# Kernel tuning notes

Hardware: AMD Instinct MI355X
Metric: run time of the kernel (lower is better)

Reference implementation:

```python
import jax, jax.numpy as jnp
import numpy as np

N_EMBD = 768
N_EXPERTS = 8
TOP_K = 2
D_FF = 4 * N_EMBD


def setup_inputs() -> dict:
    key = jax.random.key(0)
    k1, k2, k3, k4 = jax.random.split(key, 4)
    x = jax.random.normal(k1, (2, 2048, N_EMBD), dtype=jnp.float32)
    gate_w = jax.random.normal(k2, (N_EMBD, N_EXPERTS), dtype=jnp.float32) * (1.0 / np.sqrt(N_EMBD))
    w_fc = jax.random.normal(k3, (N_EXPERTS, N_EMBD, D_FF), dtype=jnp.float32) * (1.0 / np.sqrt(N_EMBD))
    w_proj = jax.random.normal(k4, (N_EXPERTS, D_FF, N_EMBD), dtype=jnp.float32) * (1.0 / np.sqrt(D_FF))
    return {"x": x, "gate_w": gate_w, "w_fc": w_fc, "w_proj": w_proj}


def reference(x, gate_w, w_fc, w_proj):
    B, S, D = x.shape
    E = w_fc.shape[0]
    xt = x.reshape(-1, D)                    # [T, D]
    T = xt.shape[0]
    scores = xt @ gate_w                      # [T, E]
    expert_weights, expert_indices = jax.lax.top_k(scores, TOP_K)  # [T, K]
    expert_weights = jax.nn.softmax(expert_weights, axis=-1)
    # per-token combine weight for each expert (0 if expert not selected)
    comb = jnp.zeros((T, E), dtype=xt.dtype)
    comb = comb.at[jnp.arange(T)[:, None], expert_indices].add(expert_weights)  # [T, E]
    out = jnp.zeros_like(xt)
    for e in range(E):  # fixed small loop over experts
        h = jax.nn.gelu(xt @ w_fc[e], approximate=False)  # torch nn.GELU default = exact erf
        y_e = h @ w_proj[e]                               # [T, D]
        out = out + comb[:, e:e + 1] * y_e
    return out.reshape(B, S, D)
```

## Files before the change

kernel.cpp:

```cpp
#include <hip/hip_runtime.h>
#include <hip/hip_bf16.h>
#include <math.h>

#define T_TOK 4096
#define D_EMB 768
#define DFF   3072
#define N_EXP 8
#define MAXT  72
#define CNTS  16

typedef __attribute__((ext_vector_type(8))) short bf16x8;
typedef __attribute__((ext_vector_type(4))) float f32x4;

typedef __attribute__((address_space(3))) unsigned int lds_u32_t;
typedef __attribute__((address_space(1))) unsigned int glob_u32_t;

__device__ __forceinline__ void gload16(const void* g, void* l) {
  __builtin_amdgcn_global_load_lds((const glob_u32_t*)g, (lds_u32_t*)l, 16, 0, 0);
}

__device__ __forceinline__ short f2bf(float f) {
  union { __hip_bfloat16 b; short s; } u;
  u.b = __float2bfloat16(f);
  return u.s;
}

__device__ __forceinline__ float gelu_f(float v) {
  float u = 0.7978845608f * v * (1.0f + 0.044715f * v * v);
  float a = fabsf(u);
  float em = __expf(-2.0f * a);
  float th = (1.0f - em) / (1.0f + em);
  th = (u < 0.0f) ? -th : th;
  return 0.5f * v * (1.0f + th);
}

__device__ __forceinline__ int swz(int row) { return (row ^ (row >> 2)) & 3; }

__global__ void zero_init_kernel(float4* __restrict__ out4, int n4, int* __restrict__ cnt) {
  int i = blockIdx.x * blockDim.x + threadIdx.x;
  if (i < N_EXP * CNTS) cnt[i] = 0;
  float4 z; z.x = z.y = z.z = z.w = 0.f;
  for (int j = i; j < n4; j += gridDim.x * blockDim.x) out4[j] = z;
}

__global__ __launch_bounds__(256)
void slab_weights(const float* __restrict__ src, short* __restrict__ dst,
                  int Kt, int Nt, int NCT, int NKTall) {
  __shared__ float t32[32][132];
  int ct = blockIdx.x, kt = blockIdx.y, e = blockIdx.z;
  const float* s = src + ((size_t)e * Kt + kt * 32) * Nt + ct * 128;
  int tid = threadIdx.x;
#pragma unroll
  for (int p4 = 0; p4 < 4; p4++) {
    int idx = tid + p4 * 256;
    int kl = idx >> 5, c4 = idx & 31;
    float4 v = *(const float4*)&s[(size_t)kl * Nt + c4 * 4];
    t32[kl][c4 * 4 + 0] = v.x; t32[kl][c4 * 4 + 1] = v.y;
    t32[kl][c4 * 4 + 2] = v.z; t32[kl][c4 * 4 + 3] = v.w;
  }
  __syncthreads();
  short* d = dst + (((size_t)e * NCT + ct) * NKTall + kt) * 4096;
#pragma unroll
  for (int i = 0; i < 2; i++) {
    int seg = tid + i * 256;
    int row = seg >> 2, p = seg & 3;
    int q = p ^ swz(row);
    union { short sv[8]; uint4 u; } o;
#pragma unroll
    for (int j = 0; j < 8; j++) o.sv[j] = f2bf(t32[q * 8 + j][row]);
    *(uint4*)&d[(size_t)seg * 8] = o.u;
  }
}

__global__ __launch_bounds__(256)
void gate_kernel(const float* __restrict__ x, const float* __restrict__ gw,
                 int* __restrict__ cnt, int* __restrict__ tok,
                 float* __restrict__ wgt) {
  __shared__ int lcnt[N_EXP];
  __shared__ int gbase[N_EXP];
  __shared__ int le[32];
  __shared__ float lw[32];
  __shared__ int lpos[32];
  int tid = threadIdx.x, lane = tid & 63, wid = tid >> 6;
  if (tid < N_EXP) lcnt[tid] = 0;
  __syncthreads();

#pragma unroll
  for (int i = 0; i < 4; i++) {
    int t = blockIdx.x * 16 + wid * 4 + i;
    float s[N_EXP];
#pragma unroll
    for (int e = 0; e < N_EXP; e++) s[e] = 0.f;
#pragma unroll
    for (int dd = 0; dd < D_EMB / 64; dd++) {
      int d = dd * 64 + lane;
      float xv = x[(size_t)t * D_EMB + d];
#pragma unroll
      for (int e = 0; e < N_EXP; e++) s[e] += xv * gw[d * N_EXP + e];
    }
#pragma unroll
    for (int e = 0; e < N_EXP; e++) {
#pragma unroll
      for (int off = 32; off > 0; off >>= 1) s[e] += __shfl_xor(s[e], off, 64);
    }
    if (lane == 0) {
      int e0 = 0;
#pragma unroll
      for (int e = 1; e < N_EXP; e++) if (s[e] > s[e0]) e0 = e;
      int e1 = -1;
#pragma unroll
      for (int e = 0; e < N_EXP; e++) {
        if (e == e0) continue;
        if (e1 < 0 || s[e] > s[e1]) e1 = e;
      }
      float p1 = __expf(s[e1] - s[e0]);
      float inv = 1.f / (1.f + p1);
      int idx = (wid * 4 + i) * 2;
      le[idx] = e0; lw[idx] = inv;           lpos[idx] = atomicAdd(&lcnt[e0], 1);
      le[idx + 1] = e1; lw[idx + 1] = p1 * inv; lpos[idx + 1] = atomicAdd(&lcnt[e1], 1);
    }
  }
  __syncthreads();
  if (tid < N_EXP) gbase[tid] = atomicAdd(&cnt[tid * CNTS], lcnt[tid]);
  __syncthreads();
  if (tid < 32) {
    int e = le[tid];
    int t = blockIdx.x * 16 + (tid >> 1);
    int p = gbase[e] + lpos[tid];
    tok[e * T_TOK + p] = t;
    wgt[e * T_TOK + p] = lw[tid];
  }
}

__global__ void plan_kernel(const int* __restrict__ cnt, int* __restrict__ offs,
                            int* __restrict__ tile_e, int* __restrict__ tile_rt,
                            int* __restrict__ ntiles) {
  if (threadIdx.x != 0 || blockIdx.x != 0) return;
  int o = 0, nt = 0;
  for (int e = 0; e < N_EXP; e++) {
    offs[e] = o;
    int tc = (cnt[e * CNTS] + 127) >> 7;
    for (int i = 0; i < tc; i++) { tile_e[nt] = e; tile_rt[nt] = i; nt++; }
    o += cnt[e * CNTS];
  }
  *ntiles = nt;
}

__global__ __launch_bounds__(256)
void gatherA_kernel(const float* __restrict__ x, const int* __restrict__ tok,
                    const int* __restrict__ cnt, const int* __restrict__ offs,
                    const int* __restrict__ tile_e, const int* __restrict__ tile_rt,
                    const int* __restrict__ ntiles, short* __restrict__ aslab) {
  int tile = blockIdx.x, kt = blockIdx.y;
  if (tile >= *ntiles) return;
  int e = tile_e[tile], rt = tile_rt[tile];
  int ne = cnt[e * CNTS];
  int tid = threadIdx.x;
  short* d = aslab + ((size_t)tile * 24 + kt) * 4096;
#pragma unroll
  for (int i = 0; i < 2; i++) {
    int seg = tid + i * 256;
    int row = seg >> 2, p = seg & 3;
    int q = p ^ swz(row);
    int r = rt * 128 + row; if (r >= ne) r = ne - 1;
    int t = tok[e * T_TOK + r];
    const float* src = x + (size_t)t * D_EMB + kt * 32 + q * 8;
    union { short sv[8]; uint4 u; } o;
#pragma unroll
    for (int j = 0; j < 8; j++) o.sv[j] = f2bf(src[j]);
    *(uint4*)&d[(size_t)seg * 8] = o.u;
  }
}

template<int KDIM, int NDIM, int SPLITK, int GRT, int GCT, int EPI>
__global__ __launch_bounds__(256, 4)
void moe_gemm(const short* __restrict__ Aop, const short* __restrict__ Bslab,
              const int* __restrict__ tok, const float* __restrict__ wgt,
              const int* __restrict__ cnt, const int* __restrict__ offs,
              const int* __restrict__ tile_e, const int* __restrict__ tile_rt,
              const int* __restrict__ ntiles,
              short* __restrict__ hout, float* __restrict__ fout) {
  const int COLT = NDIM / 128;
  const int KS = KDIM / SPLITK;
  const int NKT = KS / 32;
  const int NKTALL = KDIM / 32;
  const int BPS = GRT * GCT;
  const int NCG = COLT / GCT;
  const int PER_SK = MAXT * COLT;

  int nwg = gridDim.x;
  int cpx = nwg >> 3;
  int logical = (blockIdx.x & 7) * cpx + (blockIdx.x >> 3);
  int sk = logical / PER_SK;
  int rem = logical % PER_SK;
  int super = rem / BPS, inner = rem % BPS;
  int band = super / NCG, cg = super % NCG;
  int tile = band * GRT + (inner % GRT);
  int ct = cg * GCT + (inner / GRT);
  if (tile >= *ntiles) return;
  int e = tile_e[tile], rt = tile_rt[tile];
  int ne = cnt[e * CNTS];
  int base = offs[e];

  __shared__ __align__(16) short As[2][128 * 32];
  __shared__ __align__(16) short Bs[2][128 * 32];

  int tid = threadIdx.x;
  int lane = tid & 63;
  int wid = tid >> 6;

  const int AKT = (EPI == 0) ? 4096 : 32;
  const short* aptr[2];
  const short* bptr[2];
  int lofs[2];
#pragma unroll
  for (int i = 0; i < 2; i++) {
    int seg = tid + i * 256;
    int row = seg >> 2, p = seg & 3;
    int q = p ^ swz(row);
    if (EPI == 0) {
      aptr[i] = Aop + ((size_t)tile * 24) * 4096 + seg * 8;
    } else {
      int r = rt * 128 + row; if (r >= ne) r = ne - 1;
      aptr[i] = Aop + (size_t)(base + r) * KDIM + sk * KS + q * 8;
    }
    bptr[i] = Bslab + (((size_t)e * COLT + ct) * NKTALL + sk * NKT) * 4096 + seg * 8;
    lofs[i] = seg * 8;
  }

  f32x4 acc[4][4];
#pragma unroll
  for (int m = 0; m < 4; m++)
#pragma unroll
    for (int n = 0; n < 4; n++) acc[m][n] = (f32x4){0.f, 0.f, 0.f, 0.f};

  int wr = (wid >> 1) * 64, wc = (wid & 1) * 64;

#pragma unroll
  for (int i = 0; i < 2; i++) {
    gload16(aptr[i], &As[0][lofs[i]]);
    gload16(bptr[i], &Bs[0][lofs[i]]);
  }
  __syncthreads();

  int cur = 0;
  for (int kt = 0; kt < NKT; ++kt) {
    if (kt + 1 < NKT) {
#pragma unroll
      for (int i = 0; i < 2; i++) {
        gload16(aptr[i] + (size_t)(kt + 1) * AKT, &As[cur ^ 1][lofs[i]]);
        gload16(bptr[i] + (size_t)(kt + 1) * 4096, &Bs[cur ^ 1][lofs[i]]);
      }
    }
    int cb = lane >> 4;
    bf16x8 af[4], bv[4];
#pragma unroll
    for (int m = 0; m < 4; m++) {
      int row = wr + m * 16 + (lane & 15);
      af[m] = *(const bf16x8*)&As[cur][row * 32 + ((cb ^ swz(row)) * 8)];
    }
#pragma unroll
    for (int n = 0; n < 4; n++) {
      int row = wc + n * 16 + (lane & 15);
      bv[n] = *(const bf16x8*)&Bs[cur][row * 32 + ((cb ^ swz(row)) * 8)];
    }
#pragma unroll
    for (int m = 0; m < 4; m++)
#pragma unroll
      for (int n = 0; n < 4; n++)
        acc[m][n] = __builtin_amdgcn_mfma_f32_16x16x32_bf16(af[m], bv[n], acc[m][n], 0, 0, 0);
    __syncthreads();
    cur ^= 1;
  }

  int colbase = ct * 128 + wc;
#pragma unroll
  for (int m = 0; m < 4; m++) {
#pragma unroll
    for (int j = 0; j < 4; j++) {
      int rloc = rt * 128 + wr + m * 16 + ((lane >> 4) << 2) + j;
      if (rloc < ne) {
        if (EPI == 0) {
          size_t hrow = (size_t)(base + rloc) * NDIM;
#pragma unroll
          for (int n = 0; n < 4; n++)
            hout[hrow + colbase + n * 16 + (lane & 15)] = f2bf(gelu_f(acc[m][n][j]));
        } else {
          int t = tok[e * T_TOK + rloc];
          float w = wgt[e * T_TOK + rloc];
          float* orow = fout + (size_t)t * NDIM + colbase + (lane & 15);
#pragma unroll
          for (int n = 0; n < 4; n++)
            atomicAdd(orow + n * 16, w * acc[m][n][j]);
        }
      }
    }
  }
}

extern "C" void kernel_launch(void* const* d_in, const int* in_sizes, int n_in,
                              void* d_out, int out_size, void* d_ws, size_t ws_size,
                              hipStream_t stream) {
  const float* x   = (const float*)d_in[0];
  const float* gw  = (const float*)d_in[1];
  const float* wfc = (const float*)d_in[2];
  const float* wpj = (const float*)d_in[3];
  float* out = (float*)d_out;

  char* ws = (char*)d_ws;
  const size_t SZ_ASLAB = (size_t)MAXT * 24 * 4096 * 2;
  const size_t SZ_BFC   = (size_t)N_EXP * 24 * 24 * 4096 * 2;
  const size_t SZ_BPJ   = (size_t)N_EXP * 6 * 96 * 4096 * 2;
  const size_t SZ_H     = (size_t)2 * T_TOK * DFF * 2;
  short* aslab = (short*)(ws);
  short* bfc   = (short*)(ws + SZ_ASLAB);
  short* bpj   = (short*)(ws + SZ_ASLAB + SZ_BFC);
  short* h     = (short*)(ws + SZ_ASLAB + SZ_BFC + SZ_BPJ);
  char* p2     = ws + SZ_ASLAB + SZ_BFC + SZ_BPJ + SZ_H;
  int*   tok  = (int*)(p2);
  float* wgt  = (float*)(p2 + (size_t)N_EXP * T_TOK * 4);
  char* p3    = p2 + (size_t)N_EXP * T_TOK * 8;
  int*   cnt     = (int*)(p3);
  int*   offs    = (int*)(p3 + 1024);
  int*   tile_e  = (int*)(p3 + 1024 + 64);
  int*   tile_rt = (int*)(p3 + 1024 + 64 + 512);
  int*   ntiles  = (int*)(p3 + 1024 + 64 + 1024);

  int n4 = out_size / 4;
  zero_init_kernel<<<2048, 256, 0, stream>>>((float4*)out, n4, cnt);
  slab_weights<<<dim3(24, 24, N_EXP), 256, 0, stream>>>(wfc, bfc, D_EMB, DFF, 24, 24);
  slab_weights<<<dim3(6, 96, N_EXP), 256, 0, stream>>>(wpj, bpj, DFF, D_EMB, 6, 96);
  gate_kernel<<<T_TOK / 16, 256, 0, stream>>>(x, gw, cnt, tok, wgt);
  plan_kernel<<<1, 1, 0, stream>>>(cnt, offs, tile_e, tile_rt, ntiles);
  gatherA_kernel<<<dim3(MAXT, 24), 256, 0, stream>>>(x, tok, cnt, offs, tile_e, tile_rt, ntiles, aslab);
  moe_gemm<D_EMB, DFF, 1, 8, 8, 0><<<MAXT * (DFF / 128), 256, 0, stream>>>(
      aslab, bfc, tok, wgt, cnt, offs, tile_e, tile_rt, ntiles, h, nullptr);
  moe_gemm<DFF, D_EMB, 2, 8, 6, 1><<<2 * MAXT * (D_EMB / 128), 256, 0, stream>>>(
      h, bpj, tok, wgt, cnt, offs, tile_e, tile_rt, ntiles, nullptr, out);
}
```

Before: 219.9 us.

## Load GEMM fragments directly from swizzled slabs into registers, bypassing LDS

The grouped GEMM no longer stages tiles through LDS with global_load_lds and barriers. Each lane now loads its MFMA fragments straight from global memory, which works because the operands are pre-laid-out in tiled, swizzled slabs, and loads are double-buffered in registers. The first GEMM's epilogue writes GELU output into the same slab layout so the second GEMM can read it the same way. The MFMA operands are swapped, so the accumulator is transposed and the down-projection atomics are rearranged to match, and occupancy bounds drop to 3. This removes LDS traffic and barriers, but every wave reloads shared tiles from global or L2 without reuse through LDS, which risks higher memory traffic.

```diff
diff --git a/kernel.cpp b/kernel.cpp
--- a/kernel.cpp
+++ b/kernel.cpp
@@ -11,13 +11,6 @@
 
 typedef __attribute__((ext_vector_type(8))) short bf16x8;
 typedef __attribute__((ext_vector_type(4))) float f32x4;
-
-typedef __attribute__((address_space(3))) unsigned int lds_u32_t;
-typedef __attribute__((address_space(1))) unsigned int glob_u32_t;
-
-__device__ __forceinline__ void gload16(const void* g, void* l) {
-  __builtin_amdgcn_global_load_lds((const glob_u32_t*)g, (lds_u32_t*)l, 16, 0, 0);
-}
 
 __device__ __forceinline__ short f2bf(float f) {
   union { __hip_bfloat16 b; short s; } u;
@@ -173,20 +166,20 @@
 }
 
 template<int KDIM, int NDIM, int SPLITK, int GRT, int GCT, int EPI>
-__global__ __launch_bounds__(256, 4)
-void moe_gemm(const short* __restrict__ Aop, const short* __restrict__ Bslab,
+__global__ __launch_bounds__(256, 3)
+void moe_gemm(const short* __restrict__ Aslab, const short* __restrict__ Bslab,
               const int* __restrict__ tok, const float* __restrict__ wgt,
               const int* __restrict__ cnt, const int* __restrict__ offs,
               const int* __restrict__ tile_e, const int* __restrict__ tile_rt,
               const int* __restrict__ ntiles,
-              short* __restrict__ hout, float* __restrict__ fout) {
+              short* __restrict__ hslab, float* __restrict__ fout) {
   const int COLT = NDIM / 128;
-  const int KS = KDIM / SPLITK;
-  const int NKT = KS / 32;
+  const int NKT = (KDIM / SPLITK) / 32;
   const int NKTALL = KDIM / 32;
   const int BPS = GRT * GCT;
   const int NCG = COLT / GCT;
   const int PER_SK = MAXT * COLT;
+  static_assert(MAXT % GRT == 0 && COLT % GCT == 0, "supertile must divide grid");
 
   int nwg = gridDim.x;
   int cpx = nwg >> 3;
@@ -201,31 +194,27 @@
   int e = tile_e[tile], rt = tile_rt[tile];
   int ne = cnt[e * CNTS];
   int base = offs[e];
-
-  __shared__ __align__(16) short As[2][128 * 32];
-  __shared__ __align__(16) short Bs[2][128 * 32];
+  (void)base;
 
   int tid = threadIdx.x;
   int lane = tid & 63;
   int wid = tid >> 6;
-
-  const int AKT = (EPI == 0) ? 4096 : 32;
-  const short* aptr[2];
-  const short* bptr[2];
-  int lofs[2];
-#pragma unroll
-  for (int i = 0; i < 2; i++) {
-    int seg = tid + i * 256;
-    int row = seg >> 2, p = seg & 3;
-    int q = p ^ swz(row);
-    if (EPI == 0) {
-      aptr[i] = Aop + ((size_t)tile * 24) * 4096 + seg * 8;
-    } else {
-      int r = rt * 128 + row; if (r >= ne) r = ne - 1;
-      aptr[i] = Aop + (size_t)(base + r) * KDIM + sk * KS + q * 8;
-    }
-    bptr[i] = Bslab + (((size_t)e * COLT + ct) * NKTALL + sk * NKT) * 4096 + seg * 8;
-    lofs[i] = seg * 8;
+  int wr = (wid >> 1) * 64, wc = (wid & 1) * 64;
+  int cb = lane >> 4;
+
+  const short* pa[4];
+  const short* pb[4];
+#pragma unroll
+  for (int m = 0; m < 4; m++) {
+    int row = wr + m * 16 + (lane & 15);
+    int seg = row * 4 + (cb ^ swz(row));
+    pa[m] = Aslab + ((size_t)tile * NKTALL + sk * NKT) * 4096 + seg * 8;
+  }
+#pragma unroll
+  for (int n = 0; n < 4; n++) {
+    int row = wc + n * 16 + (lane & 15);
+    int seg = row * 4 + (cb ^ swz(row));
+    pb[n] = Bslab + (((size_t)e * COLT + ct) * NKTALL + sk * NKT) * 4096 + seg * 8;
   }
 
   f32x4 acc[4][4];
@@ -234,65 +223,66 @@
 #pragma unroll
     for (int n = 0; n < 4; n++) acc[m][n] = (f32x4){0.f, 0.f, 0.f, 0.f};
 
-  int wr = (wid >> 1) * 64, wc = (wid & 1) * 64;
-
-#pragma unroll
-  for (int i = 0; i < 2; i++) {
-    gload16(aptr[i], &As[0][lofs[i]]);
-    gload16(bptr[i], &Bs[0][lofs[i]]);
-  }
-  __syncthreads();
-
-  int cur = 0;
-  for (int kt = 0; kt < NKT; ++kt) {
-    if (kt + 1 < NKT) {
-#pragma unroll
-      for (int i = 0; i < 2; i++) {
-        gload16(aptr[i] + (size_t)(kt + 1) * AKT, &As[cur ^ 1][lofs[i]]);
-        gload16(bptr[i] + (size_t)(kt + 1) * 4096, &Bs[cur ^ 1][lofs[i]]);
+  bf16x8 a0[4], b0[4], a1[4], b1[4];
+
+#define LD(DA, DB, KT) do {                                                   \
+    _Pragma("unroll") for (int m_ = 0; m_ < 4; ++m_)                          \
+      DA[m_] = *(const bf16x8*)(pa[m_] + (size_t)(KT) * 4096);                \
+    _Pragma("unroll") for (int n_ = 0; n_ < 4; ++n_)                          \
+      DB[n_] = *(const bf16x8*)(pb[n_] + (size_t)(KT) * 4096);                \
+  } while (0)
+#define MM(AR, BR) do {                                                       \
+    _Pragma("unroll") for (int m_ = 0; m_ < 4; ++m_)                          \
+      _Pragma("unroll") for (int n_ = 0; n_ < 4; ++n_)                        \
+        acc[m_][n_] = __builtin_amdgcn_mfma_f32_16x16x32_bf16(                \
+            BR[n_], AR[m_], acc[m_][n_], 0, 0, 0);                            \
+  } while (0)
+
+  LD(a0, b0, 0);
+#pragma unroll 1
+  for (int kt = 0; kt + 2 < NKT; kt += 2) {
+    LD(a1, b1, kt + 1);
+    MM(a0, b0);
+    LD(a0, b0, kt + 2);
+    MM(a1, b1);
+  }
+  LD(a1, b1, NKT - 1);
+  MM(a0, b0);
+  MM(a1, b1);
+#undef LD
+#undef MM
+
+  if (EPI == 0) {
+#pragma unroll
+    for (int m = 0; m < 4; m++) {
+      int rowL = wr + m * 16 + (lane & 15);
+#pragma unroll
+      for (int n = 0; n < 4; n++) {
+        int C0 = ct * 128 + wc + n * 16 + ((lane >> 4) << 2);
+        int kt = C0 >> 5;
+        int p = ((C0 & 31) >> 3) ^ swz(rowL);
+        int seg = rowL * 4 + p;
+        short4 v;
+        v.x = f2bf(gelu_f(acc[m][n][0]));
+        v.y = f2bf(gelu_f(acc[m][n][1]));
+        v.z = f2bf(gelu_f(acc[m][n][2]));
+        v.w = f2bf(gelu_f(acc[m][n][3]));
+        *(short4*)&hslab[((size_t)tile * 96 + kt) * 4096 + seg * 8 + (C0 & 7)] = v;
       }
     }
-    int cb = lane >> 4;
-    bf16x8 af[4], bv[4];
+  } else {
 #pragma unroll
     for (int m = 0; m < 4; m++) {
-      int row = wr + m * 16 + (lane & 15);
-      af[m] = *(const bf16x8*)&As[cur][row * 32 + ((cb ^ swz(row)) * 8)];
-    }
-#pragma unroll
-    for (int n = 0; n < 4; n++) {
-      int row = wc + n * 16 + (lane & 15);
-      bv[n] = *(const bf16x8*)&Bs[cur][row * 32 + ((cb ^ swz(row)) * 8)];
-    }
-#pragma unroll
-    for (int m = 0; m < 4; m++)
-#pragma unroll
-      for (int n = 0; n < 4; n++)
-        acc[m][n] = __builtin_amdgcn_mfma_f32_16x16x32_bf16(af[m], bv[n], acc[m][n], 0, 0, 0);
-    __syncthreads();
-    cur ^= 1;
-  }
-
-  int colbase = ct * 128 + wc;
-#pragma unroll
-  for (int m = 0; m < 4; m++) {
-#pragma unroll
-    for (int j = 0; j < 4; j++) {
-      int rloc = rt * 128 + wr + m * 16 + ((lane >> 4) << 2) + j;
+      int rloc = rt * 128 + wr + m * 16 + (lane & 15);
       if (rloc < ne) {
-        if (EPI == 0) {
-          size_t hrow = (size_t)(base + rloc) * NDIM;
-#pragma unroll
-          for (int n = 0; n < 4; n++)
-            hout[hrow + colbase + n * 16 + (lane & 15)] = f2bf(gelu_f(acc[m][n][j]));
-        } else {
-          int t = tok[e * T_TOK + rloc];
-          float w = wgt[e * T_TOK + rloc];
-          float* orow = fout + (size_t)t * NDIM + colbase + (lane & 15);
-#pragma unroll
-          for (int n = 0; n < 4; n++)
-            atomicAdd(orow + n * 16, w * acc[m][n][j]);
-        }
+        int t = tok[e * T_TOK + rloc];
+        float w = wgt[e * T_TOK + rloc];
+        float* orow = fout + (size_t)t * NDIM + ct * 128 + wc + ((lane >> 4) << 2);
+#pragma unroll
+        for (int n = 0; n < 4; n++)
+#pragma unroll
+          for (int j = 0; j < 4; j++)
+            atomicAdd(orow + n * 16 + j, w * acc[m][n][j]);
       }
     }
   }
@@ -311,12 +301,12 @@
   const size_t SZ_ASLAB = (size_t)MAXT * 24 * 4096 * 2;
   const size_t SZ_BFC   = (size_t)N_EXP * 24 * 24 * 4096 * 2;
   const size_t SZ_BPJ   = (size_t)N_EXP * 6 * 96 * 4096 * 2;
-  const size_t SZ_H     = (size_t)2 * T_TOK * DFF * 2;
+  const size_t SZ_HSLAB = (size_t)MAXT * 96 * 4096 * 2;
   short* aslab = (short*)(ws);
   short* bfc   = (short*)(ws + SZ_ASLAB);
   short* bpj   = (short*)(ws + SZ_ASLAB + SZ_BFC);
-  short* h     = (short*)(ws + SZ_ASLAB + SZ_BFC + SZ_BPJ);
-  char* p2     = ws + SZ_ASLAB + SZ_BFC + SZ_BPJ + SZ_H;
+  short* hslab = (short*)(ws + SZ_ASLAB + SZ_BFC + SZ_BPJ);
+  char* p2     = ws + SZ_ASLAB + SZ_BFC + SZ_BPJ + SZ_HSLAB;
   int*   tok  = (int*)(p2);
   float* wgt  = (float*)(p2 + (size_t)N_EXP * T_TOK * 4);
   char* p3    = p2 + (size_t)N_EXP * T_TOK * 8;
@@ -334,7 +324,7 @@
   plan_kernel<<<1, 1, 0, stream>>>(cnt, offs, tile_e, tile_rt, ntiles);
   gatherA_kernel<<<dim3(MAXT, 24), 256, 0, stream>>>(x, tok, cnt, offs, tile_e, tile_rt, ntiles, aslab);
   moe_gemm<D_EMB, DFF, 1, 8, 8, 0><<<MAXT * (DFF / 128), 256, 0, stream>>>(
-      aslab, bfc, tok, wgt, cnt, offs, tile_e, tile_rt, ntiles, h, nullptr);
+      aslab, bfc, tok, wgt, cnt, offs, tile_e, tile_rt, ntiles, hslab, nullptr);
   moe_gemm<DFF, D_EMB, 2, 8, 6, 1><<<2 * MAXT * (D_EMB / 128), 256, 0, stream>>>(
-      h, bpj, tok, wgt, cnt, offs, tile_e, tile_rt, ntiles, nullptr, out);
-}
+      hslab, bpj, tok, wgt, cnt, offs, tile_e, tile_rt, ntiles, nullptr, out);
+}
```

Result: slower. 354.7 us (+61.3%).

## Add register-staged triple-buffered FC GEMM and cache-warming pass before GEMMs

Applied to the files above, without the earlier changes.

Replaces the FC GEMM, which used direct global-to-LDS loads, with a dedicated kernel. The new kernel prefetches three K-steps ahead into registers, writes them to double-buffered LDS and runs a fully unrolled schedule with explicit waitcnt and barriers, using a launch bound of 2 waves per SIMD. It also adds a warm kernel that streams the A slab and both weight slabs, so they sit in L2/MALL before the GEMMs run. The proj GEMM is split out of the templated kernel without changing its logic. The cost is higher register pressure and an extra full read pass over the slabs.

```diff
diff --git a/kernel.cpp b/kernel.cpp
--- a/kernel.cpp
+++ b/kernel.cpp
@@ -172,14 +172,158 @@
   }
 }
 
-template<int KDIM, int NDIM, int SPLITK, int GRT, int GCT, int EPI>
+__global__ void warm_kernel(const float4* __restrict__ a, int na,
+                            const float4* __restrict__ b, int nb,
+                            const float4* __restrict__ c, int nc) {
+  int stride = gridDim.x * blockDim.x;
+  int i0 = blockIdx.x * blockDim.x + threadIdx.x;
+  float4 s; s.x = s.y = s.z = s.w = 0.f;
+  for (int i = i0; i < na; i += stride) { float4 v = a[i]; s.x += v.x; s.y += v.y; s.z += v.z; s.w += v.w; }
+  for (int i = i0; i < nb; i += stride) { float4 v = b[i]; s.x += v.x; s.y += v.y; s.z += v.z; s.w += v.w; }
+  for (int i = i0; i < nc; i += stride) { float4 v = c[i]; s.x += v.x; s.y += v.y; s.z += v.z; s.w += v.w; }
+  asm volatile("" :: "v"(s.x), "v"(s.y), "v"(s.z), "v"(s.w));
+}
+
+__global__ __launch_bounds__(256, 2)
+void fc_gemm_pipe(const short* __restrict__ Aslab, const short* __restrict__ Bslab,
+                  const int* __restrict__ cnt, const int* __restrict__ offs,
+                  const int* __restrict__ tile_e, const int* __restrict__ tile_rt,
+                  const int* __restrict__ ntiles, short* __restrict__ hout) {
+  const int COLT = DFF / 128;
+  const int NKT = 24;
+  const int BPS = 8 * 8, NCG = COLT / 8;
+
+  int nwg = gridDim.x, cpx = nwg >> 3;
+  int logical = (blockIdx.x & 7) * cpx + (blockIdx.x >> 3);
+  int super = logical / BPS, inner = logical % BPS;
+  int band = super / NCG, cg = super % NCG;
+  int tile = band * 8 + (inner % 8);
+  int ct = cg * 8 + (inner / 8);
+  if (tile >= *ntiles) return;
+  int e = tile_e[tile], rt = tile_rt[tile];
+  int ne = cnt[e * CNTS];
+  int base = offs[e];
+
+  __shared__ __align__(16) short As[2][4096];
+  __shared__ __align__(16) short Bs[2][4096];
+
+  int tid = threadIdx.x, lane = tid & 63, wid = tid >> 6;
+  int wr = (wid >> 1) * 64, wc = (wid & 1) * 64;
+  int cb = lane >> 4;
+
+  const short* ap0 = Aslab + (size_t)tile * NKT * 4096 + tid * 8;
+  const short* ap1 = ap0 + 256 * 8;
+  const short* bp0 = Bslab + ((size_t)e * COLT + ct) * NKT * 4096 + tid * 8;
+  const short* bp1 = bp0 + 256 * 8;
+  int lo0 = tid * 8, lo1 = (tid + 256) * 8;
+
+  int offa[4], offb[4];
+#pragma unroll
+  for (int m = 0; m < 4; m++) {
+    int row = wr + m * 16 + (lane & 15);
+    offa[m] = row * 32 + ((cb ^ swz(row)) * 8);
+  }
+#pragma unroll
+  for (int n = 0; n < 4; n++) {
+    int row = wc + n * 16 + (lane & 15);
+    offb[n] = row * 32 + ((cb ^ swz(row)) * 8);
+  }
+
+  f32x4 acc[4][4];
+#pragma unroll
+  for (int m = 0; m < 4; m++)
+#pragma unroll
+    for (int n = 0; n < 4; n++) acc[m][n] = (f32x4){0.f, 0.f, 0.f, 0.f};
+
+  f32x4 rA0a, rA0b, rB0a, rB0b;
+  f32x4 rA1a, rA1b, rB1a, rB1b;
+  f32x4 rA2a, rA2b, rB2a, rB2b;
+
+#define LOADS(LA0, LA1, LB0, LB1, KT) do {                                    \
+    LA0 = *(const f32x4*)(ap0 + (size_t)(KT) * 4096);                         \
+    LA1 = *(const f32x4*)(ap1 + (size_t)(KT) * 4096);                         \
+    LB0 = *(const f32x4*)(bp0 + (size_t)(KT) * 4096);                         \
+    LB1 = *(const f32x4*)(bp1 + (size_t)(KT) * 4096);                         \
+  } while (0)
+#define WRITES(WA0, WA1, WB0, WB1, LW) do {                                   \
+    *(f32x4*)&As[LW][lo0] = WA0; *(f32x4*)&As[LW][lo1] = WA1;                 \
+    *(f32x4*)&Bs[LW][lo0] = WB0; *(f32x4*)&Bs[LW][lo1] = WB1;                 \
+  } while (0)
+#define COMPUTE(LR) do {                                                      \
+    bf16x8 af_[4], bv_[4];                                                    \
+    _Pragma("unroll") for (int m_ = 0; m_ < 4; ++m_)                          \
+      af_[m_] = *(const bf16x8*)&As[LR][offa[m_]];                            \
+    _Pragma("unroll") for (int n_ = 0; n_ < 4; ++n_)                          \
+      bv_[n_] = *(const bf16x8*)&Bs[LR][offb[n_]];                            \
+    _Pragma("unroll") for (int m_ = 0; m_ < 4; ++m_)                          \
+      _Pragma("unroll") for (int n_ = 0; n_ < 4; ++n_)                        \
+        acc[m_][n_] = __builtin_amdgcn_mfma_f32_16x16x32_bf16(                \
+            af_[m_], bv_[n_], acc[m_][n_], 0, 0, 0);                          \
+  } while (0)
+#define ENDSTEP() do {                                                        \
+    asm volatile("s_waitcnt lgkmcnt(0)" ::: "memory");                        \
+    __builtin_amdgcn_sched_barrier(0);                                        \
+    __builtin_amdgcn_s_barrier();                                             \
+  } while (0)
+#define STEP(LR, LW, WA0, WA1, WB0, WB1, LA0, LA1, LB0, LB1, KT, DOLD, DOWR) do { \
+    if (DOLD) LOADS(LA0, LA1, LB0, LB1, (KT));                                \
+    if (DOWR) WRITES(WA0, WA1, WB0, WB1, (LW));                               \
+    COMPUTE(LR);                                                              \
+    ENDSTEP();                                                                \
+  } while (0)
+
+  LOADS(rA0a, rA0b, rB0a, rB0b, 0);
+  LOADS(rA1a, rA1b, rB1a, rB1b, 1);
+  LOADS(rA2a, rA2b, rB2a, rB2b, 2);
+  WRITES(rA0a, rA0b, rB0a, rB0b, 0);
+  ENDSTEP();
+
+#pragma unroll 1
+  for (int g = 0; g < 3; ++g) {
+    int kb = 6 * g;
+    STEP(0, 1, rA1a, rA1b, rB1a, rB1b, rA0a, rA0b, rB0a, rB0b, kb + 3, 1, 1);
+    STEP(1, 0, rA2a, rA2b, rB2a, rB2b, rA1a, rA1b, rB1a, rB1b, kb + 4, 1, 1);
+    STEP(0, 1, rA0a, rA0b, rB0a, rB0b, rA2a, rA2b, rB2a, rB2b, kb + 5, 1, 1);
+    STEP(1, 0, rA1a, rA1b, rB1a, rB1b, rA0a, rA0b, rB0a, rB0b, kb + 6, 1, 1);
+    STEP(0, 1, rA2a, rA2b, rB2a, rB2b, rA1a, rA1b, rB1a, rB1b, kb + 7, 1, 1);
+    STEP(1, 0, rA0a, rA0b, rB0a, rB0b, rA2a, rA2b, rB2a, rB2b, kb + 8, 1, 1);
+  }
+  STEP(0, 1, rA1a, rA1b, rB1a, rB1b, rA0a, rA0b, rB0a, rB0b, 21, 1, 1);
+  STEP(1, 0, rA2a, rA2b, rB2a, rB2b, rA1a, rA1b, rB1a, rB1b, 22, 1, 1);
+  STEP(0, 1, rA0a, rA0b, rB0a, rB0b, rA2a, rA2b, rB2a, rB2b, 23, 1, 1);
+  STEP(1, 0, rA1a, rA1b, rB1a, rB1b, rA0a, rA0b, rB0a, rB0b, 0, 0, 1);
+  STEP(0, 1, rA2a, rA2b, rB2a, rB2b, rA1a, rA1b, rB1a, rB1b, 0, 0, 1);
+  STEP(1, 0, rA0a, rA0b, rB0a, rB0b, rA2a, rA2b, rB2a, rB2b, 0, 0, 0);
+
+#undef STEP
+#undef ENDSTEP
+#undef COMPUTE
+#undef WRITES
+#undef LOADS
+
+  int colbase = ct * 128 + wc;
+#pragma unroll
+  for (int m = 0; m < 4; m++) {
+#pragma unroll
+    for (int j = 0; j < 4; j++) {
+      int rloc = rt * 128 + wr + m * 16 + ((lane >> 4) << 2) + j;
+      if (rloc < ne) {
+        size_t hrow = (size_t)(base + rloc) * DFF;
+#pragma unroll
+        for (int n = 0; n < 4; n++)
+          hout[hrow + colbase + n * 16 + (lane & 15)] = f2bf(gelu_f(acc[m][n][j]));
+      }
+    }
+  }
+}
+
+template<int KDIM, int NDIM, int SPLITK, int GRT, int GCT>
 __global__ __launch_bounds__(256, 4)
-void moe_gemm(const short* __restrict__ Aop, const short* __restrict__ Bslab,
-              const int* __restrict__ tok, const float* __restrict__ wgt,
-              const int* __restrict__ cnt, const int* __restrict__ offs,
-              const int* __restrict__ tile_e, const int* __restrict__ tile_rt,
-              const int* __restrict__ ntiles,
-              short* __restrict__ hout, float* __restrict__ fout) {
+void proj_gemm(const short* __restrict__ Aop, const short* __restrict__ Bslab,
+               const int* __restrict__ tok, const float* __restrict__ wgt,
+               const int* __restrict__ cnt, const int* __restrict__ offs,
+               const int* __restrict__ tile_e, const int* __restrict__ tile_rt,
+               const int* __restrict__ ntiles, float* __restrict__ fout) {
   const int COLT = NDIM / 128;
   const int KS = KDIM / SPLITK;
   const int NKT = KS / 32;
@@ -188,8 +332,7 @@
   const int NCG = COLT / GCT;
   const int PER_SK = MAXT * COLT;
 
-  int nwg = gridDim.x;
-  int cpx = nwg >> 3;
+  int nwg = gridDim.x, cpx = nwg >> 3;
   int logical = (blockIdx.x & 7) * cpx + (blockIdx.x >> 3);
   int sk = logical / PER_SK;
   int rem = logical % PER_SK;
@@ -205,11 +348,8 @@
   __shared__ __align__(16) short As[2][128 * 32];
   __shared__ __align__(16) short Bs[2][128 * 32];
 
-  int tid = threadIdx.x;
-  int lane = tid & 63;
-  int wid = tid >> 6;
-
-  const int AKT = (EPI == 0) ? 4096 : 32;
+  int tid = threadIdx.x, lane = tid & 63, wid = tid >> 6;
+
   const short* aptr[2];
   const short* bptr[2];
   int lofs[2];
@@ -218,12 +358,8 @@
     int seg = tid + i * 256;
     int row = seg >> 2, p = seg & 3;
     int q = p ^ swz(row);
-    if (EPI == 0) {
-      aptr[i] = Aop + ((size_t)tile * 24) * 4096 + seg * 8;
-    } else {
-      int r = rt * 128 + row; if (r >= ne) r = ne - 1;
-      aptr[i] = Aop + (size_t)(base + r) * KDIM + sk * KS + q * 8;
-    }
+    int r = rt * 128 + row; if (r >= ne) r = ne - 1;
+    aptr[i] = Aop + (size_t)(base + r) * KDIM + sk * KS + q * 8;
     bptr[i] = Bslab + (((size_t)e * COLT + ct) * NKTALL + sk * NKT) * 4096 + seg * 8;
     lofs[i] = seg * 8;
   }
@@ -248,7 +384,7 @@
     if (kt + 1 < NKT) {
 #pragma unroll
       for (int i = 0; i < 2; i++) {
-        gload16(aptr[i] + (size_t)(kt + 1) * AKT, &As[cur ^ 1][lofs[i]]);
+        gload16(aptr[i] + (size_t)(kt + 1) * 32, &As[cur ^ 1][lofs[i]]);
         gload16(bptr[i] + (size_t)(kt + 1) * 4096, &Bs[cur ^ 1][lofs[i]]);
       }
     }
@@ -280,19 +416,12 @@
     for (int j = 0; j < 4; j++) {
       int rloc = rt * 128 + wr + m * 16 + ((lane >> 4) << 2) + j;
       if (rloc < ne) {
-        if (EPI == 0) {
-          size_t hrow = (size_t)(base + rloc) * NDIM;
-#pragma unroll
-          for (int n = 0; n < 4; n++)
-            hout[hrow + colbase + n * 16 + (lane & 15)] = f2bf(gelu_f(acc[m][n][j]));
-        } else {
-          int t = tok[e * T_TOK + rloc];
-          float w = wgt[e * T_TOK + rloc];
-          float* orow = fout + (size_t)t * NDIM + colbase + (lane & 15);
-#pragma unroll
-          for (int n = 0; n < 4; n++)
-            atomicAdd(orow + n * 16, w * acc[m][n][j]);
-        }
+        int t = tok[e * T_TOK + rloc];
+        float w = wgt[e * T_TOK + rloc];
+        float* orow = fout + (size_t)t * NDIM + colbase + (lane & 15);
+#pragma unroll
+        for (int n = 0; n < 4; n++)
+          atomicAdd(orow + n * 16, w * acc[m][n][j]);
       }
     }
   }
@@ -333,8 +462,12 @@
   gate_kernel<<<T_TOK / 16, 256, 0, stream>>>(x, gw, cnt, tok, wgt);
   plan_kernel<<<1, 1, 0, stream>>>(cnt, offs, tile_e, tile_rt, ntiles);
   gatherA_kernel<<<dim3(MAXT, 24), 256, 0, stream>>>(x, tok, cnt, offs, tile_e, tile_rt, ntiles, aslab);
-  moe_gemm<D_EMB, DFF, 1, 8, 8, 0><<<MAXT * (DFF / 128), 256, 0, stream>>>(
-      aslab, bfc, tok, wgt, cnt, offs, tile_e, tile_rt, ntiles, h, nullptr);
-  moe_gemm<DFF, D_EMB, 2, 8, 6, 1><<<2 * MAXT * (D_EMB / 128), 256, 0, stream>>>(
-      h, bpj, tok, wgt, cnt, offs, tile_e, tile_rt, ntiles, nullptr, out);
-}
+  warm_kernel<<<2048, 256, 0, stream>>>(
+      (const float4*)aslab, (int)(SZ_ASLAB / 16),
+      (const float4*)bfc,   (int)(SZ_BFC / 16),
+      (const float4*)bpj,   (int)(SZ_BPJ / 16));
+  fc_gemm_pipe<<<MAXT * (DFF / 128), 256, 0, stream>>>(
+      aslab, bfc, cnt, offs, tile_e, tile_rt, ntiles, h);
+  proj_gemm<DFF, D_EMB, 2, 8, 6><<<2 * MAXT * (D_EMB / 128), 256, 0, stream>>>(
+      h, bpj, tok, wgt, cnt, offs, tile_e, tile_rt, ntiles, out);
+}
```

New measurement: 230.6 us. 1.05x slower.

## Replace direct-to-LDS loads with register-staged three-deep prefetch pipeline in MoE GEMMs

Applied to the files above, without the earlier changes.

Both MoE GEMMs drop global_load_lds double buffering. They now prefetch three k-tiles ahead into registers, write them into a double-buffered LDS, and end each step with a manual waitcnt and barrier. The aim is to hide global-memory latency behind more outstanding loads and to precompute the LDS fragment offsets. This costs extra VGPRs, so launch bounds drop from 4 to 2 waves per SIMD, and the schedule adds a static requirement that NKT be a multiple of 6.

```diff
diff --git a/kernel.cpp b/kernel.cpp
--- a/kernel.cpp
+++ b/kernel.cpp
@@ -11,13 +11,6 @@
 
 typedef __attribute__((ext_vector_type(8))) short bf16x8;
 typedef __attribute__((ext_vector_type(4))) float f32x4;
-
-typedef __attribute__((address_space(3))) unsigned int lds_u32_t;
-typedef __attribute__((address_space(1))) unsigned int glob_u32_t;
-
-__device__ __forceinline__ void gload16(const void* g, void* l) {
-  __builtin_amdgcn_global_load_lds((const glob_u32_t*)g, (lds_u32_t*)l, 16, 0, 0);
-}
 
 __device__ __forceinline__ short f2bf(float f) {
   union { __hip_bfloat16 b; short s; } u;
@@ -173,23 +166,24 @@
 }
 
 template<int KDIM, int NDIM, int SPLITK, int GRT, int GCT, int EPI>
-__global__ __launch_bounds__(256, 4)
-void moe_gemm(const short* __restrict__ Aop, const short* __restrict__ Bslab,
-              const int* __restrict__ tok, const float* __restrict__ wgt,
-              const int* __restrict__ cnt, const int* __restrict__ offs,
-              const int* __restrict__ tile_e, const int* __restrict__ tile_rt,
-              const int* __restrict__ ntiles,
-              short* __restrict__ hout, float* __restrict__ fout) {
+__global__ __launch_bounds__(256, 2)
+void pipe_gemm(const short* __restrict__ Aop, const short* __restrict__ Bslab,
+               const int* __restrict__ tok, const float* __restrict__ wgt,
+               const int* __restrict__ cnt, const int* __restrict__ offs,
+               const int* __restrict__ tile_e, const int* __restrict__ tile_rt,
+               const int* __restrict__ ntiles,
+               short* __restrict__ hout, float* __restrict__ fout) {
   const int COLT = NDIM / 128;
   const int KS = KDIM / SPLITK;
   const int NKT = KS / 32;
   const int NKTALL = KDIM / 32;
+  const int ASTRIDE = (EPI == 0) ? 4096 : 32;
   const int BPS = GRT * GCT;
   const int NCG = COLT / GCT;
   const int PER_SK = MAXT * COLT;
-
-  int nwg = gridDim.x;
-  int cpx = nwg >> 3;
+  static_assert(NKT % 6 == 0 && NKT >= 12, "depth-3 pipeline needs NKT%6==0");
+
+  int nwg = gridDim.x, cpx = nwg >> 3;
   int logical = (blockIdx.x & 7) * cpx + (blockIdx.x >> 3);
   int sk = logical / PER_SK;
   int rem = logical % PER_SK;
@@ -202,30 +196,48 @@
   int ne = cnt[e * CNTS];
   int base = offs[e];
 
-  __shared__ __align__(16) short As[2][128 * 32];
-  __shared__ __align__(16) short Bs[2][128 * 32];
-
-  int tid = threadIdx.x;
-  int lane = tid & 63;
-  int wid = tid >> 6;
-
-  const int AKT = (EPI == 0) ? 4096 : 32;
-  const short* aptr[2];
-  const short* bptr[2];
-  int lofs[2];
-#pragma unroll
-  for (int i = 0; i < 2; i++) {
-    int seg = tid + i * 256;
-    int row = seg >> 2, p = seg & 3;
-    int q = p ^ swz(row);
-    if (EPI == 0) {
-      aptr[i] = Aop + ((size_t)tile * 24) * 4096 + seg * 8;
-    } else {
+  __shared__ __align__(16) short As[2][4096];
+  __shared__ __align__(16) short Bs[2][4096];
+
+  int tid = threadIdx.x, lane = tid & 63, wid = tid >> 6;
+  int wr = (wid >> 1) * 64, wc = (wid & 1) * 64;
+  int cb = lane >> 4;
+
+  const short* ap0;
+  const short* ap1;
+  if (EPI == 0) {
+    ap0 = Aop + (size_t)tile * NKTALL * 4096 + tid * 8;
+    ap1 = ap0 + 2048;
+  } else {
+    {
+      int seg = tid;
+      int row = seg >> 2, p = seg & 3;
+      int q = p ^ swz(row);
       int r = rt * 128 + row; if (r >= ne) r = ne - 1;
-      aptr[i] = Aop + (size_t)(base + r) * KDIM + sk * KS + q * 8;
-    }
-    bptr[i] = Bslab + (((size_t)e * COLT + ct) * NKTALL + sk * NKT) * 4096 + seg * 8;
-    lofs[i] = seg * 8;
+      ap0 = Aop + (size_t)(base + r) * KDIM + sk * KS + q * 8;
+    }
+    {
+      int seg = tid + 256;
+      int row = seg >> 2, p = seg & 3;
+      int q = p ^ swz(row);
+      int r = rt * 128 + row; if (r >= ne) r = ne - 1;
+      ap1 = Aop + (size_t)(base + r) * KDIM + sk * KS + q * 8;
+    }
+  }
+  const short* bp0 = Bslab + (((size_t)e * COLT + ct) * NKTALL + sk * NKT) * 4096 + tid * 8;
+  const short* bp1 = bp0 + 2048;
+  int lo0 = tid * 8, lo1 = (tid + 256) * 8;
+
+  int offa[4], offb[4];
+#pragma unroll
+  for (int m = 0; m < 4; m++) {
+    int row = wr + m * 16 + (lane & 15);
+    offa[m] = row * 32 + ((cb ^ swz(row)) * 8);
+  }
+#pragma unroll
+  for (int n = 0; n < 4; n++) {
+    int row = wc + n * 16 + (lane & 15);
+    offb[n] = row * 32 + ((cb ^ swz(row)) * 8);
   }
 
   f32x4 acc[4][4];
@@ -234,44 +246,71 @@
 #pragma unroll
     for (int n = 0; n < 4; n++) acc[m][n] = (f32x4){0.f, 0.f, 0.f, 0.f};
 
-  int wr = (wid >> 1) * 64, wc = (wid & 1) * 64;
-
-#pragma unroll
-  for (int i = 0; i < 2; i++) {
-    gload16(aptr[i], &As[0][lofs[i]]);
-    gload16(bptr[i], &Bs[0][lofs[i]]);
-  }
-  __syncthreads();
-
-  int cur = 0;
-  for (int kt = 0; kt < NKT; ++kt) {
-    if (kt + 1 < NKT) {
-#pragma unroll
-      for (int i = 0; i < 2; i++) {
-        gload16(aptr[i] + (size_t)(kt + 1) * AKT, &As[cur ^ 1][lofs[i]]);
-        gload16(bptr[i] + (size_t)(kt + 1) * 4096, &Bs[cur ^ 1][lofs[i]]);
-      }
-    }
-    int cb = lane >> 4;
-    bf16x8 af[4], bv[4];
-#pragma unroll
-    for (int m = 0; m < 4; m++) {
-      int row = wr + m * 16 + (lane & 15);
-      af[m] = *(const bf16x8*)&As[cur][row * 32 + ((cb ^ swz(row)) * 8)];
-    }
-#pragma unroll
-    for (int n = 0; n < 4; n++) {
-      int row = wc + n * 16 + (lane & 15);
-      bv[n] = *(const bf16x8*)&Bs[cur][row * 32 + ((cb ^ swz(row)) * 8)];
-    }
-#pragma unroll
-    for (int m = 0; m < 4; m++)
-#pragma unroll
-      for (int n = 0; n < 4; n++)
-        acc[m][n] = __builtin_amdgcn_mfma_f32_16x16x32_bf16(af[m], bv[n], acc[m][n], 0, 0, 0);
-    __syncthreads();
-    cur ^= 1;
-  }
+  f32x4 rA0a, rA0b, rB0a, rB0b;
+  f32x4 rA1a, rA1b, rB1a, rB1b;
+  f32x4 rA2a, rA2b, rB2a, rB2b;
+
+#define LOADS(LA0, LA1, LB0, LB1, KT) do {                                    \
+    LA0 = *(const f32x4*)(ap0 + (size_t)(KT) * ASTRIDE);                      \
+    LA1 = *(const f32x4*)(ap1 + (size_t)(KT) * ASTRIDE);                      \
+    LB0 = *(const f32x4*)(bp0 + (size_t)(KT) * 4096);                        \
+    LB1 = *(const f32x4*)(bp1 + (size_t)(KT) * 4096);                        \
+  } while (0)
+#define WRITES(WA0, WA1, WB0, WB1, LW) do {                                   \
+    *(f32x4*)&As[LW][lo0] = WA0; *(f32x4*)&As[LW][lo1] = WA1;                 \
+    *(f32x4*)&Bs[LW][lo0] = WB0; *(f32x4*)&Bs[LW][lo1] = WB1;                 \
+  } while (0)
+#define COMPUTE(LR) do {                                                      \
+    bf16x8 af_[4], bv_[4];                                                    \
+    _Pragma("unroll") for (int m_ = 0; m_ < 4; ++m_)                          \
+      af_[m_] = *(const bf16x8*)&As[LR][offa[m_]];                            \
+    _Pragma("unroll") for (int n_ = 0; n_ < 4; ++n_)                          \
+      bv_[n_] = *(const bf16x8*)&Bs[LR][offb[n_]];                            \
+    _Pragma("unroll") for (int m_ = 0; m_ < 4; ++m_)                          \
+      _Pragma("unroll") for (int n_ = 0; n_ < 4; ++n_)                        \
+        acc[m_][n_] = __builtin_amdgcn_mfma_f32_16x16x32_bf16(                \
+            af_[m_], bv_[n_], acc[m_][n_], 0, 0, 0);                          \
+  } while (0)
+#define ENDSTEP() do {                                                        \
+    asm volatile("s_waitcnt lgkmcnt(0)" ::: "memory");                        \
+    __builtin_amdgcn_sched_barrier(0);                                        \
+    __builtin_amdgcn_s_barrier();                                             \
+  } while (0)
+#define STEP(LR, LW, WA0, WA1, WB0, WB1, LA0, LA1, LB0, LB1, KT, DOLD, DOWR) do { \
+    if (DOLD) LOADS(LA0, LA1, LB0, LB1, (KT));                                \
+    if (DOWR) WRITES(WA0, WA1, WB0, WB1, (LW));                               \
+    COMPUTE(LR);                                                              \
+    ENDSTEP();                                                                \
+  } while (0)
+
+  LOADS(rA0a, rA0b, rB0a, rB0b, 0);
+  LOADS(rA1a, rA1b, rB1a, rB1b, 1);
+  LOADS(rA2a, rA2b, rB2a, rB2b, 2);
+  WRITES(rA0a, rA0b, rB0a, rB0b, 0);
+  ENDSTEP();
+
+#pragma unroll 1
+  for (int g = 0; g < NKT / 6 - 1; ++g) {
+    int kb = 6 * g;
+    STEP(0, 1, rA1a, rA1b, rB1a, rB1b, rA0a, rA0b, rB0a, rB0b, kb + 3, 1, 1);
+    STEP(1, 0, rA2a, rA2b, rB2a, rB2b, rA1a, rA1b, rB1a, rB1b, kb + 4, 1, 1);
+    STEP(0, 1, rA0a, rA0b, rB0a, rB0b, rA2a, rA2b, rB2a, rB2b, kb + 5, 1, 1);
+    STEP(1, 0, rA1a, rA1b, rB1a, rB1b, rA0a, rA0b, rB0a, rB0b, kb + 6, 1, 1);
+    STEP(0, 1, rA2a, rA2b, rB2a, rB2b, rA1a, rA1b, rB1a, rB1b, kb + 7, 1, 1);
+    STEP(1, 0, rA0a, rA0b, rB0a, rB0b, rA2a, rA2b, rB2a, rB2b, kb + 8, 1, 1);
+  }
+  STEP(0, 1, rA1a, rA1b, rB1a, rB1b, rA0a, rA0b, rB0a, rB0b, NKT - 3, 1, 1);
+  STEP(1, 0, rA2a, rA2b, rB2a, rB2b, rA1a, rA1b, rB1a, rB1b, NKT - 2, 1, 1);
+  STEP(0, 1, rA0a, rA0b, rB0a, rB0b, rA2a, rA2b, rB2a, rB2b, NKT - 1, 1, 1);
+  STEP(1, 0, rA1a, rA1b, rB1a, rB1b, rA0a, rA0b, rB0a, rB0b, 0, 0, 1);
+  STEP(0, 1, rA2a, rA2b, rB2a, rB2b, rA1a, rA1b, rB1a, rB1b, 0, 0, 1);
+  STEP(1, 0, rA0a, rA0b, rB0a, rB0b, rA2a, rA2b, rB2a, rB2b, 0, 0, 0);
+
+#undef STEP
+#undef ENDSTEP
+#undef COMPUTE
+#undef WRITES
+#undef LOADS
 
   int colbase = ct * 128 + wc;
 #pragma unroll
@@ -333,8 +372,8 @@
   gate_kernel<<<T_TOK / 16, 256, 0, stream>>>(x, gw, cnt, tok, wgt);
   plan_kernel<<<1, 1, 0, stream>>>(cnt, offs, tile_e, tile_rt, ntiles);
   gatherA_kernel<<<dim3(MAXT, 24), 256, 0, stream>>>(x, tok, cnt, offs, tile_e, tile_rt, ntiles, aslab);
-  moe_gemm<D_EMB, DFF, 1, 8, 8, 0><<<MAXT * (DFF / 128), 256, 0, stream>>>(
+  pipe_gemm<D_EMB, DFF, 1, 8, 8, 0><<<MAXT * (DFF / 128), 256, 0, stream>>>(
       aslab, bfc, tok, wgt, cnt, offs, tile_e, tile_rt, ntiles, h, nullptr);
-  moe_gemm<DFF, D_EMB, 2, 8, 6, 1><<<2 * MAXT * (D_EMB / 128), 256, 0, stream>>>(
+  pipe_gemm<DFF, D_EMB, 2, 8, 6, 1><<<2 * MAXT * (D_EMB / 128), 256, 0, stream>>>(
       h, bpj, tok, wgt, cnt, offs, tile_e, tile_rt, ntiles, nullptr, out);
 }
```

New measurement: 215.2 us (median of 3 runs). 1.02x faster.
